# Optimization experiments

Hardware: AMD Instinct MI355X
Metric: run time of the kernel (lower is better)

The kernel has to match this reference:

```python
import jax, jax.numpy as jnp
import numpy as np

B, IN, V, H, OUT = 4096, 1024, 48, 512, 64

def setup_inputs() -> dict:
    key = jax.random.key(0)
    ks = jax.random.split(key, 6)
    s = 0.02
    x = jax.random.normal(ks[0], (B, IN), dtype=jnp.float32)
    # stacked per-vocab MLP params: hidden layers have bias, last layer bias=False
    W1 = jax.random.normal(ks[1], (V, IN, H), dtype=jnp.float32) * s
    b1 = jax.random.normal(ks[2], (V, H), dtype=jnp.float32) * s
    W2 = jax.random.normal(ks[3], (V, H, H), dtype=jnp.float32) * s
    b2 = jax.random.normal(ks[4], (V, H), dtype=jnp.float32) * s
    W3 = jax.random.normal(ks[5], (V, H, OUT), dtype=jnp.float32) * s
    return {"x": x, "W1": W1, "b1": b1, "W2": W2, "b2": b2, "W3": W3}

def reference(x, W1, b1, W2, b2, W3):
    # grouped GEMM over the vocab axis; equivalent to the per-MLP loop + cat
    h = jax.nn.relu(jnp.einsum('bi,vih->bvh', x, W1) + b1)      # [B, V, H]
    h = jax.nn.relu(jnp.einsum('bvh,vhk->bvk', h, W2) + b2)     # [B, V, H]
    o = jnp.einsum('bvk,vko->bvo', h, W3)                        # [B, V, OUT]
    # torch.cat([...], dim=-1) == reshape since outputs are in vocab order
    return o.reshape(x.shape[0], V * OUT)
```

## Files before the change

### kernel.cpp

```cpp
#include <hip/hip_runtime.h>

#define B_SZ   4096
#define IN_SZ  1024
#define V_SZ   48
#define H_SZ   512
#define OUT_SZ 64

typedef __attribute__((ext_vector_type(4))) float f32x4;
typedef __attribute__((ext_vector_type(8))) short bf16x8;
typedef __attribute__((ext_vector_type(4))) short short4v;
typedef __attribute__((ext_vector_type(4))) float float4v;

__device__ __forceinline__ short f2bf(float f){
    unsigned u = __builtin_bit_cast(unsigned, f);
    u += 0x7fffu + ((u >> 16) & 1u);
    return (short)(u >> 16);
}

__device__ __forceinline__ void gl2lds16(const void* g, void* l){
    __builtin_amdgcn_global_load_lds(
        (const __attribute__((address_space(1))) void*)g,
        (__attribute__((address_space(3))) void*)l, 16, 0, 0);
}

#define MFMA_B16(d, a, b) d = __builtin_amdgcn_mfma_f32_16x16x32_bf16(a, b, d, 0, 0, 0)

__global__ void k_convert_x(const float* __restrict__ x, short* __restrict__ xb){
    int i = blockIdx.x * 256 + threadIdx.x;
    float4v f = ((const float4v*)x)[i];
    short4v o = { f2bf(f.x), f2bf(f.y), f2bf(f.z), f2bf(f.w) };
    ((short4v*)xb)[i] = o;
}

__global__ __launch_bounds__(256) void k_transpose_cvt4(
    const float* __restrict__ in, short* __restrict__ out, int R, int C)
{
    __shared__ short t[64][68];
    int v  = blockIdx.z;
    int c0 = blockIdx.x * 64, r0 = blockIdx.y * 64;
    int tid = threadIdx.x;
    size_t base = (size_t)v * R * C;
    const float* inp = in + base + (size_t)r0 * C + c0;
    int g    = tid >> 4;
    int col4 = (tid & 15) * 4;
    #pragma unroll
    for (int p = 0; p < 4; ++p){
        int row = p*16 + g;
        float4v f = *(const float4v*)&inp[(size_t)row * C + col4];
        short4v s = { f2bf(f.x), f2bf(f.y), f2bf(f.z), f2bf(f.w) };
        *(short4v*)&t[row][col4] = s;
    }
    __syncthreads();
    short* outp = out + base + (size_t)c0 * R + r0;
    int r4 = (tid & 15) * 4;
    #pragma unroll
    for (int p = 0; p < 4; ++p){
        int c = p*16 + g;
        short4v s = { t[r4+0][c], t[r4+1][c], t[r4+2][c], t[r4+3][c] };
        *(short4v*)&outp[(size_t)c * R + r4] = s;
    }
}

#define G1_TILE (256*64)
#define G1_NT   (IN_SZ/64)

__global__ __launch_bounds__(512) void k_gemm1(
    const short* __restrict__ xb, const short* __restrict__ W1t,
    const float* __restrict__ b1, short* __restrict__ h1)
{
    __shared__ __align__(16) short As[2*G1_TILE];
    __shared__ __align__(16) short Bs[2*G1_TILE];
    const int tid  = threadIdx.x;
    const int lane = tid & 63, wave = tid >> 6;
    const int l15  = lane & 15, quad = lane >> 4;
    const int wm = wave >> 2, wn = wave & 3;
    const int M0 = blockIdx.x * 256;
    const int N0 = blockIdx.y * 256;
    const int v  = blockIdx.z;

    const short* apan = xb  + (size_t)M0 * IN_SZ;
    const short* bpan = W1t + ((size_t)v * H_SZ + N0) * IN_SZ;

    const int lr    = tid >> 3;
    const int toff  = lr * IN_SZ + (((tid & 7) ^ (lr & 7)) * 8);
    const int wbase = tid & ~63;

    auto stage = [&](const short* pan, short* lbase, int h, int j, int t){
        gl2lds16(pan + (size_t)(h*128 + j*64) * IN_SZ + t*64 + toff,
                 lbase + (h*1024 + j*512 + wbase) * 8);
    };
    auto stage_half = [&](const short* pan, short* lbase, int h, int t){
        stage(pan, lbase, h, 0, t);
        stage(pan, lbase, h, 1, t);
    };

    stage_half(apan, As, 0, 0); stage_half(apan, As, 1, 0);
    stage_half(bpan, Bs, 0, 0); stage_half(bpan, Bs, 1, 0);
    stage_half(apan, As + G1_TILE, 0, 1); stage_half(apan, As + G1_TILE, 1, 1);
    asm volatile("s_waitcnt vmcnt(4)" ::: "memory");
    __builtin_amdgcn_s_barrier();

    f32x4 acc[8][4];
    #pragma unroll
    for (int i = 0; i < 8; ++i)
        #pragma unroll
        for (int j = 0; j < 4; ++j) acc[i][j] = (f32x4){0.f,0.f,0.f,0.f};

    const int x7 = l15 & 7;
    const int abase = (wm*128 + l15) * 64;
    const int bbase = (wn*64  + l15) * 64;
    const int c_kk0 = ((quad)     ^ x7) * 8;
    const int c_kk1 = ((quad + 4) ^ x7) * 8;

    #pragma unroll 2
    for (int t = 0; t < G1_NT; ++t){
        short* Ac = As + (t & 1) * G1_TILE;
        short* Bc = Bs + (t & 1) * G1_TILE;
        short* Bn = Bs + ((t + 1) & 1) * G1_TILE;

        bf16x8 a0[8], a1[8];

        #pragma unroll
        for (int rf = 0; rf < 8; ++rf)
            a0[rf] = *(const bf16x8*)&Ac[abase + rf*1024 + c_kk0];
        bf16x8 b00 = *(const bf16x8*)&Bc[bbase + 0*1024 + c_kk0];
        bf16x8 b01 = *(const bf16x8*)&Bc[bbase + 1*1024 + c_kk0];
        if (t + 1 < G1_NT) stage_half(bpan, Bn, 0, t + 1);
        __builtin_amdgcn_s_barrier();
        asm volatile("s_waitcnt lgkmcnt(0)" ::: "memory");
        __builtin_amdgcn_s_setprio(1);
        #pragma unroll
        for (int rf = 0; rf < 8; ++rf){
            MFMA_B16(acc[rf][0], a0[rf], b00);
            MFMA_B16(acc[rf][1], a0[rf], b01);
        }
        __builtin_amdgcn_s_setprio(0);
        __builtin_amdgcn_s_barrier();

        #pragma unroll
        for (int rf = 0; rf < 8; ++rf)
            a1[rf] = *(const bf16x8*)&Ac[abase + rf*1024 + c_kk1];
        bf16x8 b02 = *(const bf16x8*)&Bc[bbase + 2*1024 + c_kk0];
        bf16x8 b03 = *(const bf16x8*)&Bc[bbase + 3*1024 + c_kk0];
        if (t + 1 < G1_NT) stage_half(bpan, Bn, 1, t + 1);
        __builtin_amdgcn_s_barrier();
        asm volatile("s_waitcnt lgkmcnt(0)" ::: "memory");
        __builtin_amdgcn_s_setprio(1);
        #pragma unroll
        for (int rf = 0; rf < 8; ++rf){
            MFMA_B16(acc[rf][2], a0[rf], b02);
            MFMA_B16(acc[rf][3], a0[rf], b03);
        }
        __builtin_amdgcn_s_setprio(0);
        __builtin_amdgcn_s_barrier();

        bf16x8 b10 = *(const bf16x8*)&Bc[bbase + 0*1024 + c_kk1];
        bf16x8 b11 = *(const bf16x8*)&Bc[bbase + 1*1024 + c_kk1];
        if (t + 2 < G1_NT) stage_half(apan, Ac, 0, t + 2);
        __builtin_amdgcn_s_barrier();
        asm volatile("s_waitcnt lgkmcnt(0)" ::: "memory");
        __builtin_amdgcn_s_setprio(1);
        #pragma unroll
        for (int rf = 0; rf < 8; ++rf){
            MFMA_B16(acc[rf][0], a1[rf], b10);
            MFMA_B16(acc[rf][1], a1[rf], b11);
        }
        __builtin_amdgcn_s_setprio(0);
        __builtin_amdgcn_s_barrier();

        bf16x8 b12 = *(const bf16x8*)&Bc[bbase + 2*1024 + c_kk1];
        bf16x8 b13 = *(const bf16x8*)&Bc[bbase + 3*1024 + c_kk1];
        if (t + 2 < G1_NT) stage_half(apan, Ac, 1, t + 2);
        __builtin_amdgcn_s_barrier();
        asm volatile("s_waitcnt lgkmcnt(0)" ::: "memory");
        __builtin_amdgcn_s_setprio(1);
        #pragma unroll
        for (int rf = 0; rf < 8; ++rf){
            MFMA_B16(acc[rf][2], a1[rf], b12);
            MFMA_B16(acc[rf][3], a1[rf], b13);
        }
        __builtin_amdgcn_s_setprio(0);
        if (t + 2 < G1_NT)      { asm volatile("s_waitcnt vmcnt(4)" ::: "memory"); }
        else if (t + 1 < G1_NT) { asm volatile("s_waitcnt vmcnt(0)" ::: "memory"); }
        __builtin_amdgcn_s_barrier();
    }

    const float* bv = b1 + (size_t)v * H_SZ;
    short* cv = h1 + (size_t)v * (B_SZ*H_SZ);
    #pragma unroll
    for (int cf = 0; cf < 4; ++cf){
        int col = N0 + wn*64 + cf*16 + l15;
        float bb = bv[col];
        #pragma unroll
        for (int rf = 0; rf < 8; ++rf){
            int rowb = M0 + wm*128 + rf*16 + quad*4;
            #pragma unroll
            for (int r = 0; r < 4; ++r){
                float val = acc[rf][cf][r] + bb;
                val = val > 0.f ? val : 0.f;
                cv[(size_t)(rowb + r) * H_SZ + col] = f2bf(val);
            }
        }
    }
}

__global__ __launch_bounds__(512) void k_gemm23(
    const short* __restrict__ h, const short* __restrict__ W2t,
    const float* __restrict__ b2, const short* __restrict__ W3t,
    float* __restrict__ out)
{
    __shared__ __align__(16) short As[64*64];
    __shared__ __align__(16) short Bs[512*64];
    const int tid  = threadIdx.x;
    const int lane = tid & 63, wave = tid >> 6;
    const int l15  = lane & 15, quad = lane >> 4;
    const int M0 = blockIdx.x * 64;
    const int v  = blockIdx.y;

    const short* hv  = h   + (size_t)v * (B_SZ*H_SZ) + (size_t)M0 * H_SZ;
    const short* w2v = W2t + (size_t)v * (H_SZ*H_SZ);
    const short* w3v = W3t + (size_t)v * (OUT_SZ*H_SZ);

    const int rowT = tid >> 3;
    const int wT   = (tid & 7) ^ (rowT & 7);
    const short* asrc  = hv  + (size_t)rowT * H_SZ + wT*8;
    const short* bsrc0 = w2v + (size_t)rowT * H_SZ + wT*8;
    short* adst  = &As[(size_t)(tid & ~63) * 8];
    short* bdst0 = &Bs[(size_t)(tid & ~63) * 8];

    f32x4 acc[4][4];
    #pragma unroll
    for (int i = 0; i < 4; ++i)
        #pragma unroll
        for (int j = 0; j < 4; ++j) acc[i][j] = (f32x4){0.f,0.f,0.f,0.f};

    for (int k0 = 0; k0 < H_SZ; k0 += 64){
        gl2lds16(asrc + k0, adst);
        #pragma unroll
        for (int j = 0; j < 8; ++j)
            gl2lds16(bsrc0 + (size_t)j*(64*H_SZ) + k0, bdst0 + (size_t)j*512*8);
        __syncthreads();
        #pragma unroll
        for (int kk = 0; kk < 2; ++kk){
            bf16x8 a[4], b[4];
            #pragma unroll
            for (int tm = 0; tm < 4; ++tm){
                int m = tm*16 + l15;
                int slot = m*8 + ((kk*4 + quad) ^ (m & 7));
                a[tm] = *(const bf16x8*)&As[slot*8];
            }
            #pragma unroll
            for (int tn = 0; tn < 4; ++tn){
                int n = wave*64 + tn*16 + l15;
                int slot = n*8 + ((kk*4 + quad) ^ (n & 7));
                b[tn] = *(const bf16x8*)&Bs[slot*8];
            }
            #pragma unroll
            for (int tm = 0; tm < 4; ++tm)
                #pragma unroll
                for (int tn = 0; tn < 4; ++tn)
                    acc[tm][tn] = __builtin_amdgcn_mfma_f32_16x16x32_bf16(
                        a[tm], b[tn], acc[tm][tn], 0, 0, 0);
        }
        __syncthreads();
    }

    const float* bv = b2 + (size_t)v * H_SZ;
    #pragma unroll
    for (int tn = 0; tn < 4; ++tn){
        int col = wave*64 + tn*16 + l15;
        float bb = bv[col];
        int u = col >> 3, c7 = col & 7;
        #pragma unroll
        for (int tm = 0; tm < 4; ++tm){
            int rowb = tm*16 + quad*4;
            #pragma unroll
            for (int r = 0; r < 4; ++r){
                int row = rowb + r;
                float val = acc[tm][tn][r] + bb;
                val = val > 0.f ? val : 0.f;
                Bs[row*512 + ((u ^ (row & 7))*8) + c7] = f2bf(val);
            }
        }
    }
    __syncthreads();

    if (wave < 4){
        f32x4 acc3[4];
        #pragma unroll
        for (int i = 0; i < 4; ++i) acc3[i] = (f32x4){0.f,0.f,0.f,0.f};
        const int n3 = wave*16 + l15;
        const short* b3p = &w3v[(size_t)n3 * H_SZ + quad*8];
        #pragma unroll
        for (int kk = 0; kk < 16; ++kk){
            bf16x8 bfrag = *(const bf16x8*)&b3p[kk*32];
            int u = kk*4 + quad;
            #pragma unroll
            for (int tm = 0; tm < 4; ++tm){
                int m = tm*16 + l15;
                bf16x8 afrag = *(const bf16x8*)&Bs[m*512 + ((u ^ (m & 7))*8)];
                acc3[tm] = __builtin_amdgcn_mfma_f32_16x16x32_bf16(
                    afrag, bfrag, acc3[tm], 0, 0, 0);
            }
        }
        const int col = v*OUT_SZ + wave*16 + l15;
        #pragma unroll
        for (int tm = 0; tm < 4; ++tm){
            int rowb = M0 + tm*16 + quad*4;
            #pragma unroll
            for (int r = 0; r < 4; ++r)
                out[(size_t)(rowb + r) * (V_SZ*OUT_SZ) + col] = acc3[tm][r];
        }
    }
}

extern "C" void kernel_launch(void* const* d_in, const int* in_sizes, int n_in,
                              void* d_out, int out_size, void* d_ws, size_t ws_size,
                              hipStream_t stream)
{
    (void)in_sizes; (void)n_in; (void)out_size; (void)ws_size;
    const float* x  = (const float*)d_in[0];
    const float* W1 = (const float*)d_in[1];
    const float* b1 = (const float*)d_in[2];
    const float* W2 = (const float*)d_in[3];
    const float* b2 = (const float*)d_in[4];
    const float* W3 = (const float*)d_in[5];
    float* out = (float*)d_out;

    char* ws = (char*)d_ws;
    short* xb  = (short*)ws;  ws += (size_t)B_SZ * IN_SZ * 2;
    short* W1t = (short*)ws;  ws += (size_t)V_SZ * H_SZ * IN_SZ * 2;
    short* W2t = (short*)ws;  ws += (size_t)V_SZ * H_SZ * H_SZ * 2;
    short* W3t = (short*)ws;  ws += (size_t)V_SZ * OUT_SZ * H_SZ * 2;
    short* h1  = (short*)ws;

    k_convert_x<<<dim3(B_SZ*IN_SZ/1024), dim3(256), 0, stream>>>(x, xb);
    k_transpose_cvt4<<<dim3(H_SZ/64,  IN_SZ/64, V_SZ), dim3(256), 0, stream>>>(W1, W1t, IN_SZ, H_SZ);
    k_transpose_cvt4<<<dim3(H_SZ/64,  H_SZ/64,  V_SZ), dim3(256), 0, stream>>>(W2, W2t, H_SZ, H_SZ);
    k_transpose_cvt4<<<dim3(OUT_SZ/64,H_SZ/64,  V_SZ), dim3(256), 0, stream>>>(W3, W3t, H_SZ, OUT_SZ);

    k_gemm1 <<<dim3(B_SZ/256, H_SZ/256, V_SZ), dim3(512), 0, stream>>>(xb, W1t, b1, h1);
    k_gemm23<<<dim3(B_SZ/64, V_SZ), dim3(512), 0, stream>>>(h1, W2t, b2, W3t, out);
}
```

Before: 655.8 us.

## Enlarge gemm23 tile to 128 rows, swizzle block order, reschedule gemm1 A loads

The fused GEMM2+3 kernel now processes 128 rows per block with a 2x4 wave layout, halving W2 tile reloads per output row and letting all eight waves take part in the GEMM3 tail; LDS grows to a single 128KB buffer. Both GEMM kernels use a 1D grid with a modulo-8 swizzle of block indices to change how blocks map across XCDs and caches. In gemm1 the second A-fragment register load moves later and both A-tile prefetch halves are issued together, reducing register pressure at the cost of a shorter prefetch lead. The larger LDS footprint lowers occupancy to one block per CU.

```diff
diff --git a/kernel.cpp b/kernel.cpp
--- a/kernel.cpp
+++ b/kernel.cpp
@@ -63,6 +63,7 @@
 
 #define G1_TILE (256*64)
 #define G1_NT   (IN_SZ/64)
+#define G1_NBLK (16*2*V_SZ)
 
 __global__ __launch_bounds__(512) void k_gemm1(
     const short* __restrict__ xb, const short* __restrict__ W1t,
@@ -74,9 +75,12 @@
     const int lane = tid & 63, wave = tid >> 6;
     const int l15  = lane & 15, quad = lane >> 4;
     const int wm = wave >> 2, wn = wave & 3;
-    const int M0 = blockIdx.x * 256;
-    const int N0 = blockIdx.y * 256;
-    const int v  = blockIdx.z;
+
+    const int bid = blockIdx.x;
+    const int swz = (bid & 7) * (G1_NBLK/8) + (bid >> 3);
+    const int M0 = (swz & 15) * 256;
+    const int N0 = ((swz >> 4) & 1) * 256;
+    const int v  = swz >> 5;
 
     const short* apan = xb  + (size_t)M0 * IN_SZ;
     const short* bpan = W1t + ((size_t)v * H_SZ + N0) * IN_SZ;
@@ -118,8 +122,7 @@
         short* Bc = Bs + (t & 1) * G1_TILE;
         short* Bn = Bs + ((t + 1) & 1) * G1_TILE;
 
-        bf16x8 a0[8], a1[8];
-
+        bf16x8 a0[8];
         #pragma unroll
         for (int rf = 0; rf < 8; ++rf)
             a0[rf] = *(const bf16x8*)&Ac[abase + rf*1024 + c_kk0];
@@ -137,9 +140,6 @@
         __builtin_amdgcn_s_setprio(0);
         __builtin_amdgcn_s_barrier();
 
-        #pragma unroll
-        for (int rf = 0; rf < 8; ++rf)
-            a1[rf] = *(const bf16x8*)&Ac[abase + rf*1024 + c_kk1];
         bf16x8 b02 = *(const bf16x8*)&Bc[bbase + 2*1024 + c_kk0];
         bf16x8 b03 = *(const bf16x8*)&Bc[bbase + 3*1024 + c_kk0];
         if (t + 1 < G1_NT) stage_half(bpan, Bn, 1, t + 1);
@@ -154,9 +154,12 @@
         __builtin_amdgcn_s_setprio(0);
         __builtin_amdgcn_s_barrier();
 
+        bf16x8 a1[8];
+        #pragma unroll
+        for (int rf = 0; rf < 8; ++rf)
+            a1[rf] = *(const bf16x8*)&Ac[abase + rf*1024 + c_kk1];
         bf16x8 b10 = *(const bf16x8*)&Bc[bbase + 0*1024 + c_kk1];
         bf16x8 b11 = *(const bf16x8*)&Bc[bbase + 1*1024 + c_kk1];
-        if (t + 2 < G1_NT) stage_half(apan, Ac, 0, t + 2);
         __builtin_amdgcn_s_barrier();
         asm volatile("s_waitcnt lgkmcnt(0)" ::: "memory");
         __builtin_amdgcn_s_setprio(1);
@@ -170,7 +173,10 @@
 
         bf16x8 b12 = *(const bf16x8*)&Bc[bbase + 2*1024 + c_kk1];
         bf16x8 b13 = *(const bf16x8*)&Bc[bbase + 3*1024 + c_kk1];
-        if (t + 2 < G1_NT) stage_half(apan, Ac, 1, t + 2);
+        if (t + 2 < G1_NT){
+            stage_half(apan, Ac, 0, t + 2);
+            stage_half(apan, Ac, 1, t + 2);
+        }
         __builtin_amdgcn_s_barrier();
         asm volatile("s_waitcnt lgkmcnt(0)" ::: "memory");
         __builtin_amdgcn_s_setprio(1);
@@ -203,19 +209,26 @@
         }
     }
 }
+
+#define G23_NBLK ((B_SZ/128)*V_SZ)
 
 __global__ __launch_bounds__(512) void k_gemm23(
     const short* __restrict__ h, const short* __restrict__ W2t,
     const float* __restrict__ b2, const short* __restrict__ W3t,
     float* __restrict__ out)
 {
-    __shared__ __align__(16) short As[64*64];
-    __shared__ __align__(16) short Bs[512*64];
+    __shared__ __align__(16) short smem[128*512];
+    short* As = smem;
+    short* Bs = smem + 128*64;
     const int tid  = threadIdx.x;
     const int lane = tid & 63, wave = tid >> 6;
     const int l15  = lane & 15, quad = lane >> 4;
-    const int M0 = blockIdx.x * 64;
-    const int v  = blockIdx.y;
+    const int wm = wave >> 2, wn = wave & 3;
+
+    const int bid = blockIdx.x;
+    const int swz = (bid & 7) * (G23_NBLK/8) + (bid >> 3);
+    const int M0 = (swz & 31) * 128;
+    const int v  = swz >> 5;
 
     const short* hv  = h   + (size_t)v * (B_SZ*H_SZ) + (size_t)M0 * H_SZ;
     const short* w2v = W2t + (size_t)v * (H_SZ*H_SZ);
@@ -223,93 +236,97 @@
 
     const int rowT = tid >> 3;
     const int wT   = (tid & 7) ^ (rowT & 7);
-    const short* asrc  = hv  + (size_t)rowT * H_SZ + wT*8;
-    const short* bsrc0 = w2v + (size_t)rowT * H_SZ + wT*8;
-    short* adst  = &As[(size_t)(tid & ~63) * 8];
-    short* bdst0 = &Bs[(size_t)(tid & ~63) * 8];
-
-    f32x4 acc[4][4];
+    const short* asrc = hv  + (size_t)rowT * H_SZ + wT*8;
+    const short* bsrc = w2v + (size_t)rowT * H_SZ + wT*8;
+    short* adst = &As[(size_t)(tid & ~63) * 8];
+    short* bdst = &Bs[(size_t)(tid & ~63) * 8];
+
+    f32x4 acc[4][8];
     #pragma unroll
     for (int i = 0; i < 4; ++i)
         #pragma unroll
-        for (int j = 0; j < 4; ++j) acc[i][j] = (f32x4){0.f,0.f,0.f,0.f};
+        for (int j = 0; j < 8; ++j) acc[i][j] = (f32x4){0.f,0.f,0.f,0.f};
 
     for (int k0 = 0; k0 < H_SZ; k0 += 64){
-        gl2lds16(asrc + k0, adst);
+        #pragma unroll
+        for (int j = 0; j < 2; ++j)
+            gl2lds16(asrc + (size_t)j*(64*H_SZ) + k0, adst + (size_t)j*512*8);
         #pragma unroll
         for (int j = 0; j < 8; ++j)
-            gl2lds16(bsrc0 + (size_t)j*(64*H_SZ) + k0, bdst0 + (size_t)j*512*8);
+            gl2lds16(bsrc + (size_t)j*(64*H_SZ) + k0, bdst + (size_t)j*512*8);
         __syncthreads();
         #pragma unroll
         for (int kk = 0; kk < 2; ++kk){
-            bf16x8 a[4], b[4];
-            #pragma unroll
-            for (int tm = 0; tm < 4; ++tm){
-                int m = tm*16 + l15;
+            bf16x8 a[4], b[8];
+            #pragma unroll
+            for (int mf = 0; mf < 4; ++mf){
+                int m = wm*64 + mf*16 + l15;
                 int slot = m*8 + ((kk*4 + quad) ^ (m & 7));
-                a[tm] = *(const bf16x8*)&As[slot*8];
-            }
-            #pragma unroll
-            for (int tn = 0; tn < 4; ++tn){
-                int n = wave*64 + tn*16 + l15;
+                a[mf] = *(const bf16x8*)&As[slot*8];
+            }
+            #pragma unroll
+            for (int nf = 0; nf < 8; ++nf){
+                int n = wn*128 + nf*16 + l15;
                 int slot = n*8 + ((kk*4 + quad) ^ (n & 7));
-                b[tn] = *(const bf16x8*)&Bs[slot*8];
-            }
-            #pragma unroll
-            for (int tm = 0; tm < 4; ++tm)
+                b[nf] = *(const bf16x8*)&Bs[slot*8];
+            }
+            #pragma unroll
+            for (int mf = 0; mf < 4; ++mf)
                 #pragma unroll
-                for (int tn = 0; tn < 4; ++tn)
-                    acc[tm][tn] = __builtin_amdgcn_mfma_f32_16x16x32_bf16(
-                        a[tm], b[tn], acc[tm][tn], 0, 0, 0);
+                for (int nf = 0; nf < 8; ++nf)
+                    acc[mf][nf] = __builtin_amdgcn_mfma_f32_16x16x32_bf16(
+                        a[mf], b[nf], acc[mf][nf], 0, 0, 0);
         }
         __syncthreads();
     }
 
     const float* bv = b2 + (size_t)v * H_SZ;
     #pragma unroll
-    for (int tn = 0; tn < 4; ++tn){
-        int col = wave*64 + tn*16 + l15;
+    for (int nf = 0; nf < 8; ++nf){
+        int col = wn*128 + nf*16 + l15;
         float bb = bv[col];
         int u = col >> 3, c7 = col & 7;
         #pragma unroll
-        for (int tm = 0; tm < 4; ++tm){
-            int rowb = tm*16 + quad*4;
+        for (int mf = 0; mf < 4; ++mf){
+            int rowb = wm*64 + mf*16 + quad*4;
             #pragma unroll
             for (int r = 0; r < 4; ++r){
                 int row = rowb + r;
-                float val = acc[tm][tn][r] + bb;
+                float val = acc[mf][nf][r] + bb;
                 val = val > 0.f ? val : 0.f;
-                Bs[row*512 + ((u ^ (row & 7))*8) + c7] = f2bf(val);
+                smem[row*512 + ((u ^ (row & 7))*8) + c7] = f2bf(val);
             }
         }
     }
     __syncthreads();
 
-    if (wave < 4){
+    {
+        const int wm3 = wave >> 2;
+        const int wn3 = wave & 3;
         f32x4 acc3[4];
         #pragma unroll
         for (int i = 0; i < 4; ++i) acc3[i] = (f32x4){0.f,0.f,0.f,0.f};
-        const int n3 = wave*16 + l15;
+        const int n3 = wn3*16 + l15;
         const short* b3p = &w3v[(size_t)n3 * H_SZ + quad*8];
         #pragma unroll
         for (int kk = 0; kk < 16; ++kk){
             bf16x8 bfrag = *(const bf16x8*)&b3p[kk*32];
             int u = kk*4 + quad;
             #pragma unroll
-            for (int tm = 0; tm < 4; ++tm){
-                int m = tm*16 + l15;
-                bf16x8 afrag = *(const bf16x8*)&Bs[m*512 + ((u ^ (m & 7))*8)];
-                acc3[tm] = __builtin_amdgcn_mfma_f32_16x16x32_bf16(
-                    afrag, bfrag, acc3[tm], 0, 0, 0);
-            }
-        }
-        const int col = v*OUT_SZ + wave*16 + l15;
-        #pragma unroll
-        for (int tm = 0; tm < 4; ++tm){
-            int rowb = M0 + tm*16 + quad*4;
+            for (int mf = 0; mf < 4; ++mf){
+                int m = wm3*64 + mf*16 + l15;
+                bf16x8 afrag = *(const bf16x8*)&smem[m*512 + ((u ^ (m & 7))*8)];
+                acc3[mf] = __builtin_amdgcn_mfma_f32_16x16x32_bf16(
+                    afrag, bfrag, acc3[mf], 0, 0, 0);
+            }
+        }
+        const int col = v*OUT_SZ + wn3*16 + l15;
+        #pragma unroll
+        for (int mf = 0; mf < 4; ++mf){
+            int rowb = M0 + wm3*64 + mf*16 + quad*4;
             #pragma unroll
             for (int r = 0; r < 4; ++r)
-                out[(size_t)(rowb + r) * (V_SZ*OUT_SZ) + col] = acc3[tm][r];
+                out[(size_t)(rowb + r) * (V_SZ*OUT_SZ) + col] = acc3[mf][r];
         }
     }
 }
@@ -339,6 +356,6 @@
     k_transpose_cvt4<<<dim3(H_SZ/64,  H_SZ/64,  V_SZ), dim3(256), 0, stream>>>(W2, W2t, H_SZ, H_SZ);
     k_transpose_cvt4<<<dim3(OUT_SZ/64,H_SZ/64,  V_SZ), dim3(256), 0, stream>>>(W3, W3t, H_SZ, OUT_SZ);
 
-    k_gemm1 <<<dim3(B_SZ/256, H_SZ/256, V_SZ), dim3(512), 0, stream>>>(xb, W1t, b1, h1);
-    k_gemm23<<<dim3(B_SZ/64, V_SZ), dim3(512), 0, stream>>>(h1, W2t, b2, W3t, out);
-}
+    k_gemm1 <<<dim3(G1_NBLK),  dim3(512), 0, stream>>>(xb, W1t, b1, h1);
+    k_gemm23<<<dim3(G23_NBLK), dim3(512), 0, stream>>>(h1, W2t, b2, W3t, out);
+}
```

After: 714.9 us. +9.0%, slower.
